# Kernel tuning notes

Measured on AMD Instinct MI355X. Metric: run time of the kernel, lower is better.

Reference implementation:

```python
import jax, jax.numpy as jnp
import numpy as np

N_EXPERTS = 8
TOP_K = 2

def setup_inputs() -> dict:
    key = jax.random.key(0)
    k1, k2, k3, k4 = jax.random.split(key, 4)
    B, T, C, F, E = 4, 1024, 1024, 2048, N_EXPERTS
    x = jax.random.normal(k1, (B, T, C), dtype=jnp.float32)
    router_w = jax.random.normal(k2, (E, C), dtype=jnp.float32) * 0.02
    w_v = jax.random.normal(k3, (E, C, 2 * F), dtype=jnp.float32) * 0.02
    c_proj = jax.random.normal(k4, (E, F, C), dtype=jnp.float32) * 0.02
    return {"x": x, "router_w": router_w, "w_v": w_v, "c_proj": c_proj}

def reference(x, router_w, w_v, c_proj):
    B, T, C = x.shape
    E = router_w.shape[0]
    # Router: top-k softmax
    logits = jnp.einsum('btc,ec->bte', x, router_w)
    probs = jax.nn.softmax(logits, axis=-1)
    weights, indices = jax.lax.top_k(probs, TOP_K)          # [B,T,K]
    weights = weights / jnp.sum(weights, axis=-1, keepdims=True)
    avg_probs = jnp.mean(probs, axis=(0, 1))
    aux_loss = E * jnp.sum(avg_probs * avg_probs)
    # Dense per-expert SwiGLU MLP on all tokens (idiomatic jax MoE reference)
    xf = x.reshape(B * T, C)                                # [N,C]
    h = jnp.einsum('nc,ecf->enf', xf, w_v)                  # [E,N,2F]
    gate, value = jnp.split(h, 2, axis=-1)
    act = jax.nn.silu(gate) * value                         # [E,N,F]
    eo = jnp.einsum('enf,efc->nec', act, c_proj)            # [N,E,C]
    # Combine: gather each token's top-k expert outputs and weight-sum
    idx = indices.reshape(B * T, TOP_K)                     # [N,K]
    w = weights.reshape(B * T, TOP_K)                       # [N,K]
    sel = jnp.take_along_axis(eo, idx[:, :, None], axis=1)  # [N,K,C]
    out = jnp.sum(w[:, :, None] * sel, axis=1)              # [N,C]
    return out.reshape(B, T, C), aux_loss
```

## Files before the change

kernel.cpp:

```cpp
#include <hip/hip_runtime.h>
#include <hip/hip_bf16.h>
#include <stdint.h>

#define N_TOK 4096
#define C_DIM 1024
#define F_DIM 2048
#define E_NUM 8
#define SMAX 10240
#define T256_MAX 40
#define T128_MAX 72
#define RBLK 1024

typedef __attribute__((ext_vector_type(4))) float f32x4;
typedef __attribute__((ext_vector_type(8))) short s16x8;

__device__ __forceinline__ uint16_t f2bf(float f) {
    unsigned x;
    __builtin_memcpy(&x, &f, 4);
    unsigned r = (x + 0x7fffu + ((x >> 16) & 1u)) >> 16;
    return (uint16_t)r;
}
__device__ __forceinline__ float bf2f(uint16_t u) {
    unsigned v = (unsigned)u << 16;
    float f;
    __builtin_memcpy(&f, &v, 4);
    return f;
}

#define GLL16(gp, lp)                                                                  \
    __builtin_amdgcn_global_load_lds((const __attribute__((address_space(1))) unsigned int*)(gp), \
                                     (__attribute__((address_space(3))) unsigned int*)(lp), 16, 0, 0)

__global__ void router_kernel(const float* __restrict__ x, const float* __restrict__ rw,
                              int* __restrict__ topk_idx, float* __restrict__ topk_w,
                              float* __restrict__ psum_part, int* __restrict__ cnt_part) {
    __shared__ float s_p[E_NUM];
    __shared__ int s_c[E_NUM];
    if (threadIdx.x < E_NUM) { s_p[threadIdx.x] = 0.f; s_c[threadIdx.x] = 0; }
    __syncthreads();

    int lane = threadIdx.x & 63;
    int wv = threadIdx.x >> 6;
    int t = blockIdx.x * 4 + wv;

    const float* xr = x + (size_t)t * C_DIM + lane * 16;
    float xs[16];
    for (int i = 0; i < 4; i++) *(float4*)&xs[i * 4] = *(const float4*)(xr + i * 4);

    float acc[E_NUM];
    for (int e = 0; e < E_NUM; e++) {
        const float* wr = rw + e * C_DIM + lane * 16;
        float s = 0.f;
        for (int i = 0; i < 4; i++) {
            float4 v = *(const float4*)(wr + i * 4);
            s += xs[i * 4] * v.x + xs[i * 4 + 1] * v.y + xs[i * 4 + 2] * v.z + xs[i * 4 + 3] * v.w;
        }
        acc[e] = s;
    }
    for (int off = 32; off > 0; off >>= 1)
        for (int e = 0; e < E_NUM; e++) acc[e] += __shfl_down(acc[e], off, 64);

    if (lane == 0) {
        float m = acc[0];
        for (int e = 1; e < E_NUM; e++) m = fmaxf(m, acc[e]);
        float p[E_NUM], s = 0.f;
        for (int e = 0; e < E_NUM; e++) { p[e] = __expf(acc[e] - m); s += p[e]; }
        float inv = 1.f / s;
        for (int e = 0; e < E_NUM; e++) { p[e] *= inv; atomicAdd(&s_p[e], p[e]); }
        int i0 = 0;
        for (int e = 1; e < E_NUM; e++) if (p[e] > p[i0]) i0 = e;
        int i1 = (i0 == 0) ? 1 : 0;
        for (int e = 0; e < E_NUM; e++) if (e != i0 && p[e] > p[i1]) i1 = e;
        float w0 = p[i0], w1 = p[i1], wsum = w0 + w1;
        topk_idx[t * 2] = i0; topk_idx[t * 2 + 1] = i1;
        topk_w[t * 2] = w0 / wsum; topk_w[t * 2 + 1] = w1 / wsum;
        atomicAdd(&s_c[i0], 1); atomicAdd(&s_c[i1], 1);
    }
    __syncthreads();
    if (threadIdx.x < E_NUM) {
        psum_part[blockIdx.x * E_NUM + threadIdx.x] = s_p[threadIdx.x];
        cnt_part[blockIdx.x * E_NUM + threadIdx.x] = s_c[threadIdx.x];
    }
}

__global__ void reduce_plan_kernel(const float* __restrict__ psum_part, const int* __restrict__ cnt_part,
                                   int* __restrict__ offsets, int* __restrict__ tile_e256,
                                   int* __restrict__ tile_r256, int* __restrict__ tile_e128,
                                   int* __restrict__ tile_r128, float* __restrict__ aux_out) {
    __shared__ float sp[256];
    __shared__ int sc[256];
    __shared__ int s_count[E_NUM];
    __shared__ float s_psum[E_NUM];
    int e = threadIdx.x >> 5, i = threadIdx.x & 31;
    float fp = 0.f; int c = 0;
    for (int j = i; j < RBLK; j += 32) { fp += psum_part[j * E_NUM + e]; c += cnt_part[j * E_NUM + e]; }
    sp[threadIdx.x] = fp; sc[threadIdx.x] = c;
    __syncthreads();
    for (int s = 16; s > 0; s >>= 1) {
        if (i < s) { sp[threadIdx.x] += sp[threadIdx.x + s]; sc[threadIdx.x] += sc[threadIdx.x + s]; }
        __syncthreads();
    }
    if (i == 0) { s_count[e] = sc[threadIdx.x]; s_psum[e] = sp[threadIdx.x]; }
    __syncthreads();
    if (threadIdx.x == 0) {
        int off = 0, t2 = 0, t1 = 0;
        for (int ee = 0; ee < E_NUM; ee++) {
            offsets[ee] = off;
            int n = s_count[ee];
            int nt2 = (n + 255) >> 8;
            for (int k = 0; k < nt2; k++) { tile_e256[t2] = ee; tile_r256[t2] = off + k * 256; t2++; }
            int nt1 = (n + 127) >> 7;
            for (int k = 0; k < nt1; k++) { tile_e128[t1] = ee; tile_r128[t1] = off + k * 128; t1++; }
            off += nt2 * 256;
        }
        offsets[E_NUM] = off;
        for (; t2 < T256_MAX; t2++) tile_e256[t2] = -1;
        for (; t1 < T128_MAX; t1++) tile_e128[t1] = -1;
        float s = 0.f;
        for (int ee = 0; ee < E_NUM; ee++) { float a = s_psum[ee] * (1.f / N_TOK); s += a * a; }
        aux_out[0] = 8.f * s;
    }
}

__global__ void assign_kernel(const int* __restrict__ topk_idx, const float* __restrict__ topk_w,
                              const int* __restrict__ offsets, int* __restrict__ count2,
                              int* __restrict__ slot_map, float* __restrict__ slot_w,
                              int* __restrict__ tok_slot) {
    __shared__ int h[E_NUM];
    __shared__ int base[E_NUM];
    if (threadIdx.x < E_NUM) h[threadIdx.x] = 0;
    __syncthreads();
    int item = blockIdx.x * 256 + threadIdx.x;
    int e = topk_idx[item];
    int rank = atomicAdd(&h[e], 1);
    __syncthreads();
    if (threadIdx.x < E_NUM)
        base[threadIdx.x] = offsets[threadIdx.x] + atomicAdd(&count2[threadIdx.x], h[threadIdx.x]);
    __syncthreads();
    int slot = base[e] + rank;
    slot_map[slot] = item;
    slot_w[slot] = topk_w[item];
    tok_slot[item] = slot;
}

__global__ void gather_kernel(const float* __restrict__ x, const int* __restrict__ slot_map,
                              uint16_t* __restrict__ x_slots) {
    int slot = blockIdx.x;
    int item = slot_map[slot];
    if (item < 0) return;
    int t = item >> 1;
    float4 v = *(const float4*)(x + (size_t)t * C_DIM + threadIdx.x * 4);
    union { uint16_t u[4]; uint2 q; } r;
    r.u[0] = f2bf(v.x); r.u[1] = f2bf(v.y); r.u[2] = f2bf(v.z); r.u[3] = f2bf(v.w);
    *(uint2*)(x_slots + (size_t)slot * C_DIM + threadIdx.x * 4) = r.q;
}

__global__ __launch_bounds__(256) void convT_kernel(const float* __restrict__ in,
                                                    uint16_t* __restrict__ out, int R, int Cc,
                                                    int remap) {
    __shared__ uint16_t s[128 * 66];
    size_t zb = (size_t)blockIdx.z * (size_t)R * Cc;
    int c0 = blockIdx.x * 64, r0 = blockIdx.y * 128;
    int cx = (threadIdx.x & 15) * 4, ry = threadIdx.x >> 4;
    for (int j = 0; j < 8; j++) {
        int r = ry + j * 16;
        float4 v = *(const float4*)(in + zb + (size_t)(r0 + r) * Cc + c0 + cx);
        uint16_t* p = &s[r * 66 + cx];
        p[0] = f2bf(v.x); p[1] = f2bf(v.y); p[2] = f2bf(v.z); p[3] = f2bf(v.w);
    }
    __syncthreads();
    int oc = threadIdx.x & 63, wseg = threadIdx.x >> 6;
    uint16_t tmp[32];
    for (int j = 0; j < 32; j++) tmp[j] = s[(wseg * 32 + j) * 66 + oc];
    int orow = c0 + oc;
    if (remap) {
        int b = orow >> 4;
        int nb = (b < 128) ? (b * 2) : ((b - 128) * 2 + 1);
        orow = nb * 16 + (orow & 15);
    }
    uint4* dst = (uint4*)(out + zb + (size_t)orow * R + r0 + wseg * 32);
    dst[0] = *(const uint4*)&tmp[0];
    dst[1] = *(const uint4*)&tmp[8];
    dst[2] = *(const uint4*)&tmp[16];
    dst[3] = *(const uint4*)&tmp[24];
}


#define A_OFF(b, h) (((b) * 2 + (h)) * 8192)
#define B_OFF(b, h) (32768 + ((b) * 2 + (h)) * 8192)

__global__ __launch_bounds__(512, 2) void gemm1_kernel(const uint16_t* __restrict__ x_slots,
                                                       const uint16_t* __restrict__ wvT,
                                                       const int* __restrict__ tile_e256,
                                                       const int* __restrict__ tile_r256,
                                                       uint16_t* __restrict__ act) {
    __shared__ uint16_t LDS[65536];
    int bid = blockIdx.x;
    int swz = (bid & 7) * 80 + (bid >> 3);
    int my = swz >> 4, j = swz & 15;
    int e = tile_e256[my];
    if (e < 0) return;
    int row0 = tile_r256[my];
    int lane = threadIdx.x & 63, v = threadIdx.x >> 6;
    int wm = v & 1, wn = v >> 1;
    const uint16_t* wvb = wvT + (size_t)e * 4096 * 1024;

    int sk = ((lane & 3) ^ ((lane >> 3) & 3)) * 8;
    int srow = v * 32 + (lane >> 2);
    const uint16_t* aSrc0 = x_slots + (size_t)(row0 + srow) * C_DIM + sk;
    const uint16_t* aSrc1 = aSrc0 + (size_t)16 * C_DIM;
    const uint16_t* bSrc0 = wvb + (size_t)(j * 256 + srow) * C_DIM + sk;
    const uint16_t* bSrc1 = bSrc0 + (size_t)16 * C_DIM;
    int cswz = ((lane >> 4) ^ ((lane >> 1) & 3)) * 8;

    f32x4 acc[8][4];
    f32x4 z4 = {0.f, 0.f, 0.f, 0.f};
#pragma unroll
    for (int m = 0; m < 8; m++)
#pragma unroll
        for (int n = 0; n < 4; n++) acc[m][n] = z4;
    s16x8 bfr[4];

#define STAGE_A(b, h, ko)                                              \
    do {                                                               \
        GLL16(aSrc0 + (ko) + (h) * 32, &LDS[A_OFF(b, h) + v * 1024]);  \
        GLL16(aSrc1 + (ko) + (h) * 32, &LDS[A_OFF(b, h) + v * 1024 + 512]); \
    } while (0)
#define STAGE_B(b, h, ko)                                              \
    do {                                                               \
        GLL16(bSrc0 + (ko) + (h) * 32, &LDS[B_OFF(b, h) + v * 1024]);  \
        GLL16(bSrc1 + (ko) + (h) * 32, &LDS[B_OFF(b, h) + v * 1024 + 512]); \
    } while (0)

#define PHASE(b, kh, mh, LB, STG, WEND)                                                        \
    do {                                                                                       \
        s16x8 af[4];                                                                           \
        _Pragma("unroll") for (int mf = 0; mf < 4; mf++)                                       \
            af[mf] = *(const s16x8*)&LDS[A_OFF(b, kh) +                                        \
                     (wm * 128 + ((mh) * 4 + mf) * 16 + (lane & 15)) * 32 + cswz];             \
        if (LB) {                                                                              \
            _Pragma("unroll") for (int nf = 0; nf < 4; nf++)                                   \
                bfr[nf] = *(const s16x8*)&LDS[B_OFF(b, kh) +                                   \
                          (wn * 64 + nf * 16 + (lane & 15)) * 32 + cswz];                      \
        }                                                                                      \
        STG;                                                                                   \
        asm volatile("s_barrier" ::: "memory");                                                \
        __builtin_amdgcn_s_setprio(1);                                                         \
        _Pragma("unroll") for (int mf = 0; mf < 4; mf++)                                       \
            _Pragma("unroll") for (int nf = 0; nf < 4; nf++)                                   \
                acc[(mh) * 4 + mf][nf] = __builtin_amdgcn_mfma_f32_16x16x32_bf16(              \
                    af[mf], bfr[nf], acc[(mh) * 4 + mf][nf], 0, 0, 0);                         \
        __builtin_amdgcn_s_setprio(0);                                                         \
        if (WEND) asm volatile("s_waitcnt vmcnt(8)" ::: "memory");                             \
        asm volatile("s_barrier" ::: "memory");                                                \
    } while (0)

    asm volatile("s_waitcnt vmcnt(0) lgkmcnt(0)" ::: "memory");
    STAGE_A(0, 0, 0); STAGE_B(0, 0, 0);
    STAGE_A(0, 1, 0); STAGE_B(0, 1, 0);
    STAGE_A(1, 0, 64); STAGE_B(1, 0, 64);
    asm volatile("s_waitcnt vmcnt(8)" ::: "memory");
    asm volatile("s_barrier" ::: "memory");

    for (int i = 0; i < 8; i++) {
        int ko1 = ((2 * i + 1) & 15) * 64;
        int ko2 = ((2 * i + 2) & 15) * 64;
        int ko3 = ((2 * i + 3) & 15) * 64;
        PHASE(0, 0, 0, 1, STAGE_A(1, 1, ko1), 0);
        PHASE(0, 0, 1, 0, STAGE_B(1, 1, ko1), 1);
        PHASE(0, 1, 0, 1, STAGE_A(0, 0, ko2), 0);
        PHASE(0, 1, 1, 0, STAGE_B(0, 0, ko2), 1);
        PHASE(1, 0, 0, 1, STAGE_A(0, 1, ko2), 0);
        PHASE(1, 0, 1, 0, STAGE_B(0, 1, ko2), 1);
        PHASE(1, 1, 0, 1, STAGE_A(1, 0, ko3), 0);
        PHASE(1, 1, 1, 0, STAGE_B(1, 0, ko3), 1);
    }

#pragma unroll
    for (int mfa = 0; mfa < 8; mfa++)
#pragma unroll
        for (int nfp = 0; nfp < 2; nfp++) {
            f32x4 g = acc[mfa][nfp * 2], vv = acc[mfa][nfp * 2 + 1];
#pragma unroll
            for (int r = 0; r < 4; r++) {
                int row = row0 + wm * 128 + mfa * 16 + (lane >> 4) * 4 + r;
                int f = j * 128 + wn * 32 + nfp * 16 + (lane & 15);
                float a = g[r] * vv[r] / (1.f + __expf(-g[r]));
                act[(size_t)row * F_DIM + f] = f2bf(a);
            }
        }
#undef STAGE_A
#undef STAGE_B
#undef PHASE
}

__global__ __launch_bounds__(256) void gemm2_kernel(const uint16_t* __restrict__ act,
                                                    const uint16_t* __restrict__ cpT,
                                                    const int* __restrict__ tile_e128,
                                                    const int* __restrict__ tile_r128,
                                                    const int* __restrict__ slot_map,
                                                    const float* __restrict__ slot_w,
                                                    uint16_t* __restrict__ eo) {
    int e = tile_e128[blockIdx.y];
    if (e < 0) return;
    int row0 = tile_r128[blockIdx.y];
    int cb = blockIdx.x * 128;
    __shared__ uint16_t As[128 * 32];
    __shared__ uint16_t Bs[128 * 32];
    int lane = threadIdx.x & 63, w = threadIdx.x >> 6;
    int wm = w & 1, wn = w >> 1;
    const uint16_t* cpb = cpT + (size_t)e * 1024 * 2048;

    int sk = (((lane & 3) ^ ((lane >> 3) & 3))) * 8;
    int ar = w * 32 + (lane >> 2);
    const uint16_t* agp0 = act + (size_t)(row0 + ar) * F_DIM + sk;
    const uint16_t* agp1 = agp0 + (size_t)16 * F_DIM;
    const uint16_t* bgp0 = cpb + (size_t)(cb + ar) * F_DIM + sk;
    const uint16_t* bgp1 = bgp0 + (size_t)16 * F_DIM;

    int cswz = ((lane >> 4) ^ ((lane >> 1) & 3)) * 8;

    f32x4 acc[4][4];
    f32x4 z4 = {0.f, 0.f, 0.f, 0.f};
    for (int mf = 0; mf < 4; mf++)
        for (int nf = 0; nf < 4; nf++) acc[mf][nf] = z4;

    for (int kt = 0; kt < 64; ++kt) {
        int ko = kt * 32;
        __syncthreads();
        GLL16(agp0 + ko, As + w * 1024);
        GLL16(agp1 + ko, As + w * 1024 + 512);
        GLL16(bgp0 + ko, Bs + w * 1024);
        GLL16(bgp1 + ko, Bs + w * 1024 + 512);
        __syncthreads();
        s16x8 af[4], bf[4];
        for (int mf = 0; mf < 4; mf++)
            af[mf] = *(const s16x8*)&As[(wm * 64 + mf * 16 + (lane & 15)) * 32 + cswz];
        for (int nf = 0; nf < 4; nf++)
            bf[nf] = *(const s16x8*)&Bs[(wn * 64 + nf * 16 + (lane & 15)) * 32 + cswz];
        for (int mf = 0; mf < 4; mf++)
            for (int nf = 0; nf < 4; nf++)
                acc[mf][nf] = __builtin_amdgcn_mfma_f32_16x16x32_bf16(af[mf], bf[nf], acc[mf][nf], 0, 0, 0);
    }
    for (int mf = 0; mf < 4; mf++)
        for (int r = 0; r < 4; r++) {
            int slotr = row0 + wm * 64 + mf * 16 + (lane >> 4) * 4 + r;
            int t2k = slot_map[slotr];
            if (t2k < 0) continue;
            float wgt = slot_w[slotr];
            for (int nf = 0; nf < 4; nf++) {
                int col = cb + wn * 64 + nf * 16 + (lane & 15);
                eo[(size_t)slotr * C_DIM + col] = f2bf(wgt * acc[mf][nf][r]);
            }
        }
}

__global__ void combine_kernel(const uint16_t* __restrict__ eo, const int* __restrict__ tok_slot,
                               float* __restrict__ out) {
    int t = blockIdx.x;
    int s0 = tok_slot[2 * t], s1 = tok_slot[2 * t + 1];
    int c = threadIdx.x * 4;
    uint2 a = *(const uint2*)(eo + (size_t)s0 * C_DIM + c);
    uint2 b = *(const uint2*)(eo + (size_t)s1 * C_DIM + c);
    float4 o;
    o.x = bf2f((uint16_t)(a.x & 0xffff)) + bf2f((uint16_t)(b.x & 0xffff));
    o.y = bf2f((uint16_t)(a.x >> 16)) + bf2f((uint16_t)(b.x >> 16));
    o.z = bf2f((uint16_t)(a.y & 0xffff)) + bf2f((uint16_t)(b.y & 0xffff));
    o.w = bf2f((uint16_t)(a.y >> 16)) + bf2f((uint16_t)(b.y >> 16));
    *(float4*)(out + (size_t)t * C_DIM + c) = o;
}

extern "C" void kernel_launch(void* const* d_in, const int* in_sizes, int n_in,
                              void* d_out, int out_size, void* d_ws, size_t ws_size,
                              hipStream_t stream) {
    (void)in_sizes; (void)n_in; (void)out_size; (void)ws_size;
    const float* x = (const float*)d_in[0];
    const float* rw = (const float*)d_in[1];
    const float* wv = (const float*)d_in[2];
    const float* cp = (const float*)d_in[3];
    float* out = (float*)d_out;

    char* ws = (char*)d_ws;
    size_t off = 0;
    auto alloc = [&](size_t sz) -> void* {
        off = (off + 255) & ~(size_t)255;
        void* p = ws + off;
        off += sz;
        return p;
    };
    uint16_t* wvT = (uint16_t*)alloc((size_t)E_NUM * 4096 * 1024 * 2);
    uint16_t* cpT = (uint16_t*)alloc((size_t)E_NUM * 1024 * 2048 * 2);
    uint16_t* x_slots = (uint16_t*)alloc((size_t)SMAX * C_DIM * 2);
    uint16_t* act = (uint16_t*)alloc((size_t)SMAX * F_DIM * 2);
    uint16_t* eo = x_slots;
    float* psum_part = (float*)alloc((size_t)RBLK * E_NUM * 4);
    int* cnt_part = (int*)alloc((size_t)RBLK * E_NUM * 4);
    int* count2 = (int*)alloc(E_NUM * 4);
    int* offsets = (int*)alloc((E_NUM + 1) * 4);
    int* tile_e256 = (int*)alloc(T256_MAX * 4);
    int* tile_r256 = (int*)alloc(T256_MAX * 4);
    int* tile_e128 = (int*)alloc(T128_MAX * 4);
    int* tile_r128 = (int*)alloc(T128_MAX * 4);
    int* topk_idx = (int*)alloc((size_t)N_TOK * 2 * 4);
    float* topk_w = (float*)alloc((size_t)N_TOK * 2 * 4);
    int* slot_map = (int*)alloc((size_t)SMAX * 4);
    float* slot_w = (float*)alloc((size_t)SMAX * 4);
    int* tok_slot = (int*)alloc((size_t)N_TOK * 2 * 4);

    hipMemsetAsync(count2, 0, E_NUM * 4, stream);
    hipMemsetAsync(slot_map, 0xFF, (size_t)SMAX * 4, stream);

    router_kernel<<<RBLK, 256, 0, stream>>>(x, rw, topk_idx, topk_w, psum_part, cnt_part);
    reduce_plan_kernel<<<1, 256, 0, stream>>>(psum_part, cnt_part, offsets, tile_e256, tile_r256,
                                              tile_e128, tile_r128, out + (size_t)N_TOK * C_DIM);
    assign_kernel<<<N_TOK * 2 / 256, 256, 0, stream>>>(topk_idx, topk_w, offsets, count2,
                                                       slot_map, slot_w, tok_slot);
    gather_kernel<<<SMAX, 256, 0, stream>>>(x, slot_map, x_slots);
    convT_kernel<<<dim3(4096 / 64, 1024 / 128, E_NUM), 256, 0, stream>>>(wv, wvT, 1024, 4096, 1);
    convT_kernel<<<dim3(1024 / 64, 2048 / 128, E_NUM), 256, 0, stream>>>(cp, cpT, 2048, 1024, 0);
    gemm1_kernel<<<16 * T256_MAX, 512, 0, stream>>>(x_slots, wvT, tile_e256, tile_r256, act);
    gemm2_kernel<<<dim3(8, T128_MAX), 256, 0, stream>>>(act, cpT, tile_e128, tile_r128,
                                                        slot_map, slot_w, eo);
    combine_kernel<<<N_TOK, 256, 0, stream>>>(eo, tok_slot, out);
}
```

Measured before the change: 486.8 us.

## Retile gemm1 to 256x128 triple-buffered tiles and fuse combine via atomics

Result: no change. 496.3 us (+1.9%).

```diff
diff --git a/kernel.cpp b/kernel.cpp
--- a/kernel.cpp
+++ b/kernel.cpp
@@ -19,12 +19,6 @@
     __builtin_memcpy(&x, &f, 4);
     unsigned r = (x + 0x7fffu + ((x >> 16) & 1u)) >> 16;
     return (uint16_t)r;
-}
-__device__ __forceinline__ float bf2f(uint16_t u) {
-    unsigned v = (unsigned)u << 16;
-    float f;
-    __builtin_memcpy(&f, &v, 4);
-    return f;
 }
 
 #define GLL16(gp, lp)                                                                  \
@@ -124,8 +118,7 @@
 
 __global__ void assign_kernel(const int* __restrict__ topk_idx, const float* __restrict__ topk_w,
                               const int* __restrict__ offsets, int* __restrict__ count2,
-                              int* __restrict__ slot_map, float* __restrict__ slot_w,
-                              int* __restrict__ tok_slot) {
+                              int* __restrict__ slot_map, float* __restrict__ slot_w) {
     __shared__ int h[E_NUM];
     __shared__ int base[E_NUM];
     if (threadIdx.x < E_NUM) h[threadIdx.x] = 0;
@@ -140,7 +133,6 @@
     int slot = base[e] + rank;
     slot_map[slot] = item;
     slot_w[slot] = topk_w[item];
-    tok_slot[item] = slot;
 }
 
 __global__ void gather_kernel(const float* __restrict__ x, const int* __restrict__ slot_map,
@@ -186,31 +178,30 @@
 }
 
 
-#define A_OFF(b, h) (((b) * 2 + (h)) * 8192)
-#define B_OFF(b, h) (32768 + ((b) * 2 + (h)) * 8192)
-
-__global__ __launch_bounds__(512, 2) void gemm1_kernel(const uint16_t* __restrict__ x_slots,
+#define A_PL(p) ((p) * 8192)
+#define B_PL(p) (24576 + (p) * 4096)
+
+__global__ __launch_bounds__(256, 2) void gemm1_kernel(const uint16_t* __restrict__ x_slots,
                                                        const uint16_t* __restrict__ wvT,
                                                        const int* __restrict__ tile_e256,
                                                        const int* __restrict__ tile_r256,
                                                        uint16_t* __restrict__ act) {
-    __shared__ uint16_t LDS[65536];
+    __shared__ uint16_t LDS[36864];
     int bid = blockIdx.x;
-    int swz = (bid & 7) * 80 + (bid >> 3);
-    int my = swz >> 4, j = swz & 15;
+    int swz = (bid & 7) * 160 + (bid >> 3);
+    int my = swz >> 5, j = swz & 31;
     int e = tile_e256[my];
     if (e < 0) return;
     int row0 = tile_r256[my];
-    int lane = threadIdx.x & 63, v = threadIdx.x >> 6;
-    int wm = v & 1, wn = v >> 1;
+    int lane = threadIdx.x & 63, w = threadIdx.x >> 6;
+    int wm = w & 1, wn = w >> 1;
     const uint16_t* wvb = wvT + (size_t)e * 4096 * 1024;
 
     int sk = ((lane & 3) ^ ((lane >> 3) & 3)) * 8;
-    int srow = v * 32 + (lane >> 2);
-    const uint16_t* aSrc0 = x_slots + (size_t)(row0 + srow) * C_DIM + sk;
-    const uint16_t* aSrc1 = aSrc0 + (size_t)16 * C_DIM;
-    const uint16_t* bSrc0 = wvb + (size_t)(j * 256 + srow) * C_DIM + sk;
-    const uint16_t* bSrc1 = bSrc0 + (size_t)16 * C_DIM;
+    int srow = w * 32 + (lane >> 2);
+    const uint16_t* aS = x_slots + (size_t)(row0 + srow) * C_DIM + sk;
+    const uint16_t* bS = wvb + (size_t)(j * 128 + srow) * C_DIM + sk;
+    int dA = w * 1024 + lane * 8;
     int cswz = ((lane >> 4) ^ ((lane >> 1) & 3)) * 8;
 
     f32x4 acc[8][4];
@@ -219,79 +210,79 @@
     for (int m = 0; m < 8; m++)
 #pragma unroll
         for (int n = 0; n < 4; n++) acc[m][n] = z4;
-    s16x8 bfr[4];
-
-#define STAGE_A(b, h, ko)                                              \
-    do {                                                               \
-        GLL16(aSrc0 + (ko) + (h) * 32, &LDS[A_OFF(b, h) + v * 1024]);  \
-        GLL16(aSrc1 + (ko) + (h) * 32, &LDS[A_OFF(b, h) + v * 1024 + 512]); \
+
+#define STAGE_A(p, ko)                                                   \
+    do {                                                                 \
+        GLL16(aS + (ko), &LDS[A_PL(p) + dA]);                            \
+        GLL16(aS + (ko) + 16 * C_DIM, &LDS[A_PL(p) + dA + 512]);         \
+        GLL16(aS + (ko) + 128 * C_DIM, &LDS[A_PL(p) + 4096 + dA]);       \
+        GLL16(aS + (ko) + 144 * C_DIM, &LDS[A_PL(p) + 4096 + dA + 512]); \
     } while (0)
-#define STAGE_B(b, h, ko)                                              \
-    do {                                                               \
-        GLL16(bSrc0 + (ko) + (h) * 32, &LDS[B_OFF(b, h) + v * 1024]);  \
-        GLL16(bSrc1 + (ko) + (h) * 32, &LDS[B_OFF(b, h) + v * 1024 + 512]); \
+#define STAGE_B(p, ko)                                                   \
+    do {                                                                 \
+        GLL16(bS + (ko), &LDS[B_PL(p) + dA]);                            \
+        GLL16(bS + (ko) + 16 * C_DIM, &LDS[B_PL(p) + dA + 512]);         \
     } while (0)
 
-#define PHASE(b, kh, mh, LB, STG, WEND)                                                        \
-    do {                                                                                       \
-        s16x8 af[4];                                                                           \
-        _Pragma("unroll") for (int mf = 0; mf < 4; mf++)                                       \
-            af[mf] = *(const s16x8*)&LDS[A_OFF(b, kh) +                                        \
-                     (wm * 128 + ((mh) * 4 + mf) * 16 + (lane & 15)) * 32 + cswz];             \
-        if (LB) {                                                                              \
-            _Pragma("unroll") for (int nf = 0; nf < 4; nf++)                                   \
-                bfr[nf] = *(const s16x8*)&LDS[B_OFF(b, kh) +                                   \
-                          (wn * 64 + nf * 16 + (lane & 15)) * 32 + cswz];                      \
-        }                                                                                      \
-        STG;                                                                                   \
-        asm volatile("s_barrier" ::: "memory");                                                \
-        __builtin_amdgcn_s_setprio(1);                                                         \
-        _Pragma("unroll") for (int mf = 0; mf < 4; mf++)                                       \
-            _Pragma("unroll") for (int nf = 0; nf < 4; nf++)                                   \
-                acc[(mh) * 4 + mf][nf] = __builtin_amdgcn_mfma_f32_16x16x32_bf16(              \
-                    af[mf], bfr[nf], acc[(mh) * 4 + mf][nf], 0, 0, 0);                         \
-        __builtin_amdgcn_s_setprio(0);                                                         \
-        if (WEND) asm volatile("s_waitcnt vmcnt(8)" ::: "memory");                             \
-        asm volatile("s_barrier" ::: "memory");                                                \
+#define KSTEP(cur, nxt, ko2, DOSTG, WN)                                                         \
+    do {                                                                                        \
+        s16x8 af0[4], af1[4], bfr[4];                                                           \
+        _Pragma("unroll") for (int mf = 0; mf < 4; mf++)                                        \
+            af0[mf] = *(const s16x8*)&LDS[A_PL(cur) + (wm * 128 + mf * 16 + (lane & 15)) * 32 + cswz]; \
+        _Pragma("unroll") for (int nf = 0; nf < 4; nf++)                                        \
+            bfr[nf] = *(const s16x8*)&LDS[B_PL(cur) + (wn * 64 + nf * 16 + (lane & 15)) * 32 + cswz];  \
+        if (DOSTG) STAGE_A(nxt, ko2);                                                           \
+        asm volatile("s_barrier" ::: "memory");                                                 \
+        __builtin_amdgcn_s_setprio(1);                                                          \
+        _Pragma("unroll") for (int mf = 0; mf < 4; mf++)                                        \
+            _Pragma("unroll") for (int nf = 0; nf < 4; nf++)                                    \
+                acc[mf][nf] = __builtin_amdgcn_mfma_f32_16x16x32_bf16(af0[mf], bfr[nf], acc[mf][nf], 0, 0, 0); \
+        __builtin_amdgcn_s_setprio(0);                                                          \
+        asm volatile("s_barrier" ::: "memory");                                                 \
+        _Pragma("unroll") for (int mf = 0; mf < 4; mf++)                                        \
+            af1[mf] = *(const s16x8*)&LDS[A_PL(cur) + (wm * 128 + (4 + mf) * 16 + (lane & 15)) * 32 + cswz]; \
+        if (DOSTG) STAGE_B(nxt, ko2);                                                           \
+        asm volatile("s_barrier" ::: "memory");                                                 \
+        __builtin_amdgcn_s_setprio(1);                                                          \
+        _Pragma("unroll") for (int mf = 0; mf < 4; mf++)                                        \
+            _Pragma("unroll") for (int nf = 0; nf < 4; nf++)                                    \
+                acc[4 + mf][nf] = __builtin_amdgcn_mfma_f32_16x16x32_bf16(af1[mf], bfr[nf], acc[4 + mf][nf], 0, 0, 0); \
+        __builtin_amdgcn_s_setprio(0);                                                          \
+        if ((WN) == 6) asm volatile("s_waitcnt vmcnt(6)" ::: "memory");                         \
+        else if ((WN) == 0) asm volatile("s_waitcnt vmcnt(0)" ::: "memory");                    \
+        asm volatile("s_barrier" ::: "memory");                                                 \
     } while (0)
 
     asm volatile("s_waitcnt vmcnt(0) lgkmcnt(0)" ::: "memory");
-    STAGE_A(0, 0, 0); STAGE_B(0, 0, 0);
-    STAGE_A(0, 1, 0); STAGE_B(0, 1, 0);
-    STAGE_A(1, 0, 64); STAGE_B(1, 0, 64);
-    asm volatile("s_waitcnt vmcnt(8)" ::: "memory");
+    STAGE_A(0, 0); STAGE_B(0, 0);
+    STAGE_A(1, 32); STAGE_B(1, 32);
+    asm volatile("s_waitcnt vmcnt(6)" ::: "memory");
     asm volatile("s_barrier" ::: "memory");
 
-    for (int i = 0; i < 8; i++) {
-        int ko1 = ((2 * i + 1) & 15) * 64;
-        int ko2 = ((2 * i + 2) & 15) * 64;
-        int ko3 = ((2 * i + 3) & 15) * 64;
-        PHASE(0, 0, 0, 1, STAGE_A(1, 1, ko1), 0);
-        PHASE(0, 0, 1, 0, STAGE_B(1, 1, ko1), 1);
-        PHASE(0, 1, 0, 1, STAGE_A(0, 0, ko2), 0);
-        PHASE(0, 1, 1, 0, STAGE_B(0, 0, ko2), 1);
-        PHASE(1, 0, 0, 1, STAGE_A(0, 1, ko2), 0);
-        PHASE(1, 0, 1, 0, STAGE_B(0, 1, ko2), 1);
-        PHASE(1, 1, 0, 1, STAGE_A(1, 0, ko3), 0);
-        PHASE(1, 1, 1, 0, STAGE_B(1, 0, ko3), 1);
-    }
+    for (int kt = 0; kt < 30; kt += 3) {
+        KSTEP(0, 2, (kt + 2) * 32, 1, 6);
+        KSTEP(1, 0, (kt + 3) * 32, 1, 6);
+        KSTEP(2, 1, (kt + 4) * 32, 1, 6);
+    }
+    KSTEP(0, 0, 0, 0, 0);
+    KSTEP(1, 0, 0, 0, -1);
 
 #pragma unroll
     for (int mfa = 0; mfa < 8; mfa++)
 #pragma unroll
-        for (int nfp = 0; nfp < 2; nfp++) {
-            f32x4 g = acc[mfa][nfp * 2], vv = acc[mfa][nfp * 2 + 1];
+        for (int p = 0; p < 2; p++) {
+            f32x4 g = acc[mfa][p * 2], vv = acc[mfa][p * 2 + 1];
 #pragma unroll
             for (int r = 0; r < 4; r++) {
                 int row = row0 + wm * 128 + mfa * 16 + (lane >> 4) * 4 + r;
-                int f = j * 128 + wn * 32 + nfp * 16 + (lane & 15);
+                int f = (j * 4 + wn * 2 + p) * 16 + (lane & 15);
                 float a = g[r] * vv[r] / (1.f + __expf(-g[r]));
                 act[(size_t)row * F_DIM + f] = f2bf(a);
             }
         }
 #undef STAGE_A
 #undef STAGE_B
-#undef PHASE
+#undef KSTEP
 }
 
 __global__ __launch_bounds__(256) void gemm2_kernel(const uint16_t* __restrict__ act,
@@ -300,7 +291,7 @@
                                                     const int* __restrict__ tile_r128,
                                                     const int* __restrict__ slot_map,
                                                     const float* __restrict__ slot_w,
-                                                    uint16_t* __restrict__ eo) {
+                                                    float* __restrict__ out) {
     int e = tile_e128[blockIdx.y];
     if (e < 0) return;
     int row0 = tile_r128[blockIdx.y];
@@ -345,29 +336,15 @@
     for (int mf = 0; mf < 4; mf++)
         for (int r = 0; r < 4; r++) {
             int slotr = row0 + wm * 64 + mf * 16 + (lane >> 4) * 4 + r;
-            int t2k = slot_map[slotr];
-            if (t2k < 0) continue;
+            int item = slot_map[slotr];
+            if (item < 0) continue;
+            int tok = item >> 1;
             float wgt = slot_w[slotr];
             for (int nf = 0; nf < 4; nf++) {
                 int col = cb + wn * 64 + nf * 16 + (lane & 15);
-                eo[(size_t)slotr * C_DIM + col] = f2bf(wgt * acc[mf][nf][r]);
+                atomicAdd(&out[(size_t)tok * C_DIM + col], wgt * acc[mf][nf][r]);
             }
         }
-}
-
-__global__ void combine_kernel(const uint16_t* __restrict__ eo, const int* __restrict__ tok_slot,
-                               float* __restrict__ out) {
-    int t = blockIdx.x;
-    int s0 = tok_slot[2 * t], s1 = tok_slot[2 * t + 1];
-    int c = threadIdx.x * 4;
-    uint2 a = *(const uint2*)(eo + (size_t)s0 * C_DIM + c);
-    uint2 b = *(const uint2*)(eo + (size_t)s1 * C_DIM + c);
-    float4 o;
-    o.x = bf2f((uint16_t)(a.x & 0xffff)) + bf2f((uint16_t)(b.x & 0xffff));
-    o.y = bf2f((uint16_t)(a.x >> 16)) + bf2f((uint16_t)(b.x >> 16));
-    o.z = bf2f((uint16_t)(a.y & 0xffff)) + bf2f((uint16_t)(b.y & 0xffff));
-    o.w = bf2f((uint16_t)(a.y >> 16)) + bf2f((uint16_t)(b.y >> 16));
-    *(float4*)(out + (size_t)t * C_DIM + c) = o;
 }
 
 extern "C" void kernel_launch(void* const* d_in, const int* in_sizes, int n_in,
@@ -392,7 +369,6 @@
     uint16_t* cpT = (uint16_t*)alloc((size_t)E_NUM * 1024 * 2048 * 2);
     uint16_t* x_slots = (uint16_t*)alloc((size_t)SMAX * C_DIM * 2);
     uint16_t* act = (uint16_t*)alloc((size_t)SMAX * F_DIM * 2);
-    uint16_t* eo = x_slots;
     float* psum_part = (float*)alloc((size_t)RBLK * E_NUM * 4);
     int* cnt_part = (int*)alloc((size_t)RBLK * E_NUM * 4);
     int* count2 = (int*)alloc(E_NUM * 4);
@@ -405,21 +381,20 @@
     float* topk_w = (float*)alloc((size_t)N_TOK * 2 * 4);
     int* slot_map = (int*)alloc((size_t)SMAX * 4);
     float* slot_w = (float*)alloc((size_t)SMAX * 4);
-    int* tok_slot = (int*)alloc((size_t)N_TOK * 2 * 4);
 
     hipMemsetAsync(count2, 0, E_NUM * 4, stream);
     hipMemsetAsync(slot_map, 0xFF, (size_t)SMAX * 4, stream);
+    hipMemsetAsync(out, 0, (size_t)N_TOK * C_DIM * 4, stream);
 
     router_kernel<<<RBLK, 256, 0, stream>>>(x, rw, topk_idx, topk_w, psum_part, cnt_part);
     reduce_plan_kernel<<<1, 256, 0, stream>>>(psum_part, cnt_part, offsets, tile_e256, tile_r256,
                                               tile_e128, tile_r128, out + (size_t)N_TOK * C_DIM);
     assign_kernel<<<N_TOK * 2 / 256, 256, 0, stream>>>(topk_idx, topk_w, offsets, count2,
-                                                       slot_map, slot_w, tok_slot);
+                                                       slot_map, slot_w);
     gather_kernel<<<SMAX, 256, 0, stream>>>(x, slot_map, x_slots);
     convT_kernel<<<dim3(4096 / 64, 1024 / 128, E_NUM), 256, 0, stream>>>(wv, wvT, 1024, 4096, 1);
     convT_kernel<<<dim3(1024 / 64, 2048 / 128, E_NUM), 256, 0, stream>>>(cp, cpT, 2048, 1024, 0);
-    gemm1_kernel<<<16 * T256_MAX, 512, 0, stream>>>(x_slots, wvT, tile_e256, tile_r256, act);
+    gemm1_kernel<<<32 * T256_MAX, 256, 0, stream>>>(x_slots, wvT, tile_e256, tile_r256, act);
     gemm2_kernel<<<dim3(8, T128_MAX), 256, 0, stream>>>(act, cpT, tile_e128, tile_r128,
-                                                        slot_map, slot_w, eo);
-    combine_kernel<<<N_TOK, 256, 0, stream>>>(eo, tok_slot, out);
-}
+                                                        slot_map, slot_w, out);
+}
```
